# Optimization experiments

Hardware: AMD Instinct MI355X
Metric: run time of the kernel (lower is better)

## Reference

```python
import jax, jax.numpy as jnp
import numpy as np

N = 16384      # total nodes (16 graphs x 1024 nodes)
PG = 1024      # nodes per graph
NB = 16        # graphs in batch
E = 131072     # edges (intra-graph)
FIN = 16       # input_dim; xy coords in cols 0,1
HID = 128      # hidden_dim
H = 4          # num_heads
DH = HID // H  # per-head dim
NLAYERS = 3
NCLS = 1
NEG_SLOPE = 0.2

# D2 views: identity, flip-x, flip-y, flip-both (signs applied to xy cols 0,1)
_signs = np.ones((4, FIN), np.float32)
_signs[1, 0] = -1.0
_signs[2, 1] = -1.0
_signs[3, 0] = -1.0
_signs[3, 1] = -1.0
VIEW_SIGNS = jnp.asarray(_signs)


def setup_inputs() -> dict:
    key = jax.random.key(0)
    ks = jax.random.split(key, 16)
    x = jax.random.normal(ks[0], (N, FIN), jnp.float32)
    # intra-graph edges: dst forced into same graph block as src (matches the
    # torch per-graph edge filtering, which drops all cross-graph edges)
    src = jax.random.randint(ks[1], (E,), 0, N, dtype=jnp.int32)
    off = jax.random.randint(ks[2], (E,), 0, PG, dtype=jnp.int32)
    dst = (src // PG) * PG + off
    edge_index = jnp.stack([src, dst], axis=0)
    batch = (jnp.arange(N, dtype=jnp.int32) // PG)

    def w(k, fi, fo):
        return (jax.random.normal(k, (fi, fo), jnp.float32) / np.sqrt(fi))

    return dict(
        x=x, edge_index=edge_index, batch=batch,
        W0l=w(ks[3], FIN, HID), W0r=w(ks[4], FIN, HID),
        a0=jax.random.normal(ks[5], (H, DH), jnp.float32) / np.sqrt(DH),
        Wres0=w(ks[6], FIN, HID),
        Wl=jax.random.normal(ks[7], (NLAYERS - 1, HID, HID), jnp.float32) / np.sqrt(HID),
        Wr=jax.random.normal(ks[8], (NLAYERS - 1, HID, HID), jnp.float32) / np.sqrt(HID),
        att=jax.random.normal(ks[9], (NLAYERS - 1, H, DH), jnp.float32) / np.sqrt(DH),
        Wh1=w(ks[10], HID, HID), bh1=jnp.zeros((HID,), jnp.float32),
        Wh2=w(ks[11], HID, NCLS), bh2=jnp.zeros((NCLS,), jnp.float32),
    )


def _gatv2_layer(h, Wlk, Wrk, a, src, dst, Wres=None, act=True):
    # GATv2: e_ij = a^T LeakyReLU(Wl h_j + Wr h_i), softmax over incoming edges of i
    hl = (h @ Wlk).reshape(-1, H, DH)   # [N,H,D] source messages
    hr = (h @ Wrk).reshape(-1, H, DH)   # [N,H,D] target queries
    s = hl[src] + hr[dst]               # [E,H,D]
    e = jnp.einsum('ehd,hd->eh', jax.nn.leaky_relu(s, NEG_SLOPE), a)  # [E,H]
    m = jax.ops.segment_max(e, dst, num_segments=N)
    ex = jnp.exp(e - m[dst])
    denom = jax.ops.segment_sum(ex, dst, num_segments=N)
    alpha = ex / (denom[dst] + 1e-16)   # [E,H] per-dst softmax
    out = jax.ops.segment_sum(alpha[..., None] * hl[src], dst, num_segments=N)
    out = out.reshape(-1, H * DH)
    res = h @ Wres if Wres is not None else h
    out = out + res
    return jax.nn.elu(out) if act else out


def _backbone(xv, src, dst, W0l, W0r, a0, Wres0, Wl, Wr, att):
    h = _gatv2_layer(xv, W0l, W0r, a0, src, dst, Wres=Wres0, act=True)
    for i in range(NLAYERS - 1):
        last = (i == NLAYERS - 2)
        h = _gatv2_layer(h, Wl[i], Wr[i], att[i], src, dst, Wres=None, act=not last)
    return h


def reference(x, edge_index, batch, W0l, W0r, a0, Wres0, Wl, Wr, att, Wh1, bh1, Wh2, bh2):
    src, dst = edge_index[0], edge_index[1]
    # 4 D2 views of node features (sign flips on xy columns); vmap over views
    x4 = x[None, :, :] * VIEW_SIGNS[:, None, :]  # [4,N,FIN]
    emb4 = jax.vmap(lambda xv: _backbone(xv, src, dst, W0l, W0r, a0, Wres0, Wl, Wr, att))(x4)  # [4,N,HID]
    node_emb = emb4.mean(axis=0)  # mean over D2 views -> [N,HID]
    logits = jax.nn.relu(node_emb @ Wh1 + bh1) @ Wh2 + bh2  # [N,NCLS]
    return logits
```

## Files before the change

kernel.cpp:

```cpp
#include <hip/hip_runtime.h>
#include <hip/hip_bf16.h>
#include <math.h>

#define NN 16384
#define EE 131072
#define FIN 16
#define HID 128
#define NEG_SLOPE 0.2f

typedef float  floatx4 __attribute__((ext_vector_type(4)));
typedef short  shortx8 __attribute__((ext_vector_type(8)));

__device__ inline unsigned bf_hi_bits(float x) {
    unsigned u = __float_as_uint(x);
    return (u + 0x7FFFu + ((u >> 16) & 1u)) >> 16;
}

__global__ void count_kernel(const int* __restrict__ dst, int* __restrict__ deg) {
    int e = blockIdx.x * 256 + threadIdx.x;
    atomicAdd(&deg[dst[e]], 1);
}

__global__ __launch_bounds__(1024) void scan_kernel(int* __restrict__ degw ,
                                                    int* __restrict__ ptr) {
    __shared__ int sums[1024];
    int t = threadIdx.x;
    int base = t * 16;
    int local[16];
    int s = 0;
#pragma unroll
    for (int i = 0; i < 16; i++) { local[i] = degw[base + i]; s += local[i]; }
    sums[t] = s;
    __syncthreads();
    for (int off = 1; off < 1024; off <<= 1) {
        int v = (t >= off) ? sums[t - off] : 0;
        __syncthreads();
        sums[t] += v;
        __syncthreads();
    }
    int ex = (t == 0) ? 0 : sums[t - 1];
#pragma unroll
    for (int i = 0; i < 16; i++) {
        ptr[base + i] = ex;
        degw[base + i] = ex;
        ex += local[i];
    }
    if (t == 1023) ptr[NN] = sums[1023];
}

__global__ void scatter_kernel(const int* __restrict__ src, const int* __restrict__ dst,
                               int* __restrict__ ptrw, int* __restrict__ csr_src) {
    int e = blockIdx.x * 256 + threadIdx.x;
    int p = atomicAdd(&ptrw[dst[e]], 1);
    csr_src[p] = src[e];
}

__global__ void wsplit_kernel(const float* __restrict__ Wl, const float* __restrict__ Wr,
                              const float* __restrict__ Wh1,
                              unsigned short* __restrict__ hi, unsigned short* __restrict__ lo) {
    int mat = blockIdx.y;
    const float* W = (mat == 0) ? Wl : (mat == 1) ? Wr : (mat == 2) ? Wl + HID * HID
                   : (mat == 3) ? Wr + HID * HID : Wh1;
    int ct = blockIdx.x;
    int t = threadIdx.x;
    int kt = t >> 6, l = t & 63;
    long obase = (((long)mat * 32 + (ct * 4 + kt)) * 64 + l) * 8;
    int c = ct * 16 + (l & 15);
    int kbase = kt * 32 + ((l >> 4) << 3);
#pragma unroll
    for (int j = 0; j < 8; j++) {
        float x = W[(kbase + j) * HID + c];
        unsigned hb = bf_hi_bits(x);
        float r = x - __uint_as_float(hb << 16);
        unsigned lb = bf_hi_bits(r);
        hi[obase + j] = (unsigned short)hb;
        lo[obase + j] = (unsigned short)lb;
    }
}

#define L0_BLOCKS 2048
__global__ __launch_bounds__(256) void l0_kernel(const float* __restrict__ x,
                                                 const float* __restrict__ W0l,
                                                 const float* __restrict__ W0r,
                                                 const float* __restrict__ Wres,
                                                 float* __restrict__ hl,
                                                 float* __restrict__ hr,
                                                 float* __restrict__ hres,
                                                 int viewBase, long totalRows) {
    int tid = threadIdx.x;
    int c2 = (tid & 63) * 2;
    float2 wl2[FIN], wr2[FIN], ws2[FIN];
#pragma unroll
    for (int k = 0; k < FIN; k++) {
        wl2[k] = *(const float2*)(W0l + k * HID + c2);
        wr2[k] = *(const float2*)(W0r + k * HID + c2);
        ws2[k] = *(const float2*)(Wres + k * HID + c2);
    }
    for (long lw = (long)blockIdx.x * 4 + (tid >> 6); lw < totalRows;
         lw += (long)L0_BLOCKS * 4) {
        int v = viewBase + (int)(lw >> 14);
        int n = (int)(lw & (NN - 1));
        const float* xr = x + (long)n * FIN;
        float al0 = 0.f, al1 = 0.f, ar0 = 0.f, ar1 = 0.f, as0 = 0.f, as1 = 0.f;
#pragma unroll
        for (int k = 0; k < FIN; k++) {
            float xk = xr[k];
            if (k == 0 && (v & 1)) xk = -xk;
            if (k == 1 && (v & 2)) xk = -xk;
            al0 += xk * wl2[k].x; al1 += xk * wl2[k].y;
            ar0 += xk * wr2[k].x; ar1 += xk * wr2[k].y;
            as0 += xk * ws2[k].x; as1 += xk * ws2[k].y;
        }
        long base = lw * HID + c2;
        *(float2*)(hl + base)   = make_float2(al0, al1);
        *(float2*)(hr + base)   = make_float2(ar0, ar1);
        *(float2*)(hres + base) = make_float2(as0, as1);
    }
}

__global__ __launch_bounds__(256) void attn_kernel(const float* __restrict__ hl,
                                                   const float* __restrict__ hr,
                                                   const float* __restrict__ res,
                                                   const int* __restrict__ ptr,
                                                   const int* __restrict__ csr_src,
                                                   const float* __restrict__ avec,
                                                   float* __restrict__ hout,
                                                   int act,
                                                   int gvPerXcd) {
    int xcd = blockIdx.x & 7;
    int slot = blockIdx.x >> 3;
    int gv = xcd * gvPerXcd + (slot >> 8);
    int within = slot & 255;
    int gw = (gv << 10) + (within << 2) + (threadIdx.x >> 6);
    int l = threadIdx.x & 63;
    int n = gw & (NN - 1);
    int col = ((l >> 4) << 5) + ((l & 15) << 1);
    long base = (long)gw * HID;
    float2 hr2 = *(const float2*)(hr + base + col);
    float2 a2 = *(const float2*)(avec + col);
    float m = -INFINITY, ssum = 0.f, acc0 = 0.f, acc1 = 0.f;
    int beg = ptr[n], end = ptr[n + 1];
    long vbase = (long)(gw >> 14) * NN * HID;
    int j = beg;
    for (; j + 1 < end; j += 2) {
        int sa = csr_src[j];
        int sb = csr_src[j + 1];
        float2 ha = *(const float2*)(hl + vbase + (long)sa * HID + col);
        float2 hb = *(const float2*)(hl + vbase + (long)sb * HID + col);
        float sa0 = ha.x + hr2.x, sa1 = ha.y + hr2.y;
        float sb0 = hb.x + hr2.x, sb1 = hb.y + hr2.y;
        float ta0 = sa0 > 0.f ? sa0 : NEG_SLOPE * sa0;
        float ta1 = sa1 > 0.f ? sa1 : NEG_SLOPE * sa1;
        float tb0 = sb0 > 0.f ? sb0 : NEG_SLOPE * sb0;
        float tb1 = sb1 > 0.f ? sb1 : NEG_SLOPE * sb1;
        float p1 = ta0 * a2.x + ta1 * a2.y;
        float p2 = tb0 * a2.x + tb1 * a2.y;
        p1 += __shfl_xor(p1, 1, 16);
        p2 += __shfl_xor(p2, 1, 16);
        p1 += __shfl_xor(p1, 2, 16);
        p2 += __shfl_xor(p2, 2, 16);
        p1 += __shfl_xor(p1, 4, 16);
        p2 += __shfl_xor(p2, 4, 16);
        p1 += __shfl_xor(p1, 8, 16);
        p2 += __shfl_xor(p2, 8, 16);
        float m12 = fmaxf(p1, p2);
        float w1 = __expf(p1 - m12);
        float w2 = __expf(p2 - m12);
        float mn = fmaxf(m, m12);
        float cold = __expf(m - mn);
        float c12 = __expf(m12 - mn);
        ssum = ssum * cold + (w1 + w2) * c12;
        acc0 = acc0 * cold + (w1 * ha.x + w2 * hb.x) * c12;
        acc1 = acc1 * cold + (w1 * ha.y + w2 * hb.y) * c12;
        m = mn;
    }
    if (j < end) {
        int sa = csr_src[j];
        float2 ha = *(const float2*)(hl + vbase + (long)sa * HID + col);
        float s0 = ha.x + hr2.x, s1 = ha.y + hr2.y;
        float t0 = s0 > 0.f ? s0 : NEG_SLOPE * s0;
        float t1 = s1 > 0.f ? s1 : NEG_SLOPE * s1;
        float p = t0 * a2.x + t1 * a2.y;
        p += __shfl_xor(p, 1, 16);
        p += __shfl_xor(p, 2, 16);
        p += __shfl_xor(p, 4, 16);
        p += __shfl_xor(p, 8, 16);
        float mn = fmaxf(m, p);
        float cold = __expf(m - mn);
        float wnew = __expf(p - mn);
        ssum = ssum * cold + wnew;
        acc0 = acc0 * cold + wnew * ha.x;
        acc1 = acc1 * cold + wnew * ha.y;
        m = mn;
    }
    float inv = 1.f / (ssum + 1e-16f);
    float2 r2 = *(const float2*)(res + base + col);
    float o0 = acc0 * inv + r2.x;
    float o1 = acc1 * inv + r2.y;
    if (act) {
        o0 = o0 > 0.f ? o0 : expm1f(o0);
        o1 = o1 > 0.f ? o1 : expm1f(o1);
    }
    *(float2*)(hout + base + col) = make_float2(o0, o1);
}

__global__ __launch_bounds__(256) void gemm_mfma(const float* __restrict__ A,
                                                 const unsigned short* __restrict__ whi,
                                                 const unsigned short* __restrict__ wlo,
                                                 int mat0, int mat1,
                                                 float* __restrict__ C0, float* __restrict__ C1,
                                                 const float* __restrict__ bias, int doRelu) {
    int mat = (blockIdx.z == 0) ? mat0 : mat1;
    float* C = (blockIdx.z == 0) ? C0 : C1;
    const unsigned short* bh = whi + (long)mat * 16384;
    const unsigned short* bl = wlo + (long)mat * 16384;
    int tid = threadIdx.x;
    int w = tid >> 6, l = tid & 63;
    int rh = w >> 1, ch = w & 1;
    long row0 = (long)blockIdx.x * 128 + rh * 64;
    int lr = l & 15;
    int lk = (l >> 4) << 3;
    floatx4 acc[4][4];
#pragma unroll
    for (int i = 0; i < 4; i++)
#pragma unroll
        for (int j = 0; j < 4; j++) acc[i][j] = (floatx4)0.f;

    for (int kt = 0; kt < 4; kt++) {
        shortx8 bhf[4], blf[4];
#pragma unroll
        for (int ctl = 0; ctl < 4; ctl++) {
            int ct = ch * 4 + ctl;
            long fi = ((long)(ct * 4 + kt) * 64 + l) * 8;
            bhf[ctl] = *(const shortx8*)(bh + fi);
            blf[ctl] = *(const shortx8*)(bl + fi);
        }
#pragma unroll
        for (int rt = 0; rt < 4; rt++) {
            const float* ap = A + (row0 + rt * 16 + lr) * HID + kt * 32 + lk;
            float4 x0 = *(const float4*)(ap);
            float4 x1 = *(const float4*)(ap + 4);
            float xs[8] = {x0.x, x0.y, x0.z, x0.w, x1.x, x1.y, x1.z, x1.w};
            shortx8 ah, al;
#pragma unroll
            for (int i = 0; i < 8; i++) {
                unsigned hb = bf_hi_bits(xs[i]);
                float r = xs[i] - __uint_as_float(hb << 16);
                unsigned lb = bf_hi_bits(r);
                ah[i] = (short)hb;
                al[i] = (short)lb;
            }
#pragma unroll
            for (int ctl = 0; ctl < 4; ctl++)
                acc[rt][ctl] = __builtin_amdgcn_mfma_f32_16x16x32_bf16(ah, bhf[ctl], acc[rt][ctl], 0, 0, 0);
#pragma unroll
            for (int ctl = 0; ctl < 4; ctl++)
                acc[rt][ctl] = __builtin_amdgcn_mfma_f32_16x16x32_bf16(ah, blf[ctl], acc[rt][ctl], 0, 0, 0);
#pragma unroll
            for (int ctl = 0; ctl < 4; ctl++)
                acc[rt][ctl] = __builtin_amdgcn_mfma_f32_16x16x32_bf16(al, bhf[ctl], acc[rt][ctl], 0, 0, 0);
        }
    }
    int lrow4 = (l >> 4) * 4;
#pragma unroll
    for (int rt = 0; rt < 4; rt++) {
#pragma unroll
        for (int ctl = 0; ctl < 4; ctl++) {
            int col = ch * 64 + ctl * 16 + lr;
            float badd = bias ? bias[col] : 0.f;
#pragma unroll
            for (int rg = 0; rg < 4; rg++) {
                long row = row0 + rt * 16 + lrow4 + rg;
                float v = acc[rt][ctl][rg] + badd;
                if (doRelu) v = fmaxf(v, 0.f);
                C[row * HID + col] = v;
            }
        }
    }
}

__global__ void acc_kernel(const float* __restrict__ h, float* __restrict__ emb, int k) {
    int i = blockIdx.x * 256 + threadIdx.x;
    const float4* h4 = (const float4*)h;
    float4 s = make_float4(0.f, 0.f, 0.f, 0.f);
    for (int lv = 0; lv < k; lv++) {
        float4 a = h4[i + (long)lv * NN * 32];
        s.x += a.x; s.y += a.y; s.z += a.z; s.w += a.w;
    }
    float4* e4 = (float4*)emb;
    float4 o = e4[i];
    o.x += 0.25f * s.x; o.y += 0.25f * s.y; o.z += 0.25f * s.z; o.w += 0.25f * s.w;
    e4[i] = o;
}

__global__ void logits_kernel(const float* __restrict__ z, const float* __restrict__ Wh2,
                              const float* __restrict__ bh2, float* __restrict__ out) {
    int w = (blockIdx.x * 256 + threadIdx.x) >> 6;
    int l = threadIdx.x & 63;
    float v = z[(long)w * HID + l] * Wh2[l] + z[(long)w * HID + 64 + l] * Wh2[64 + l];
    v += __shfl_xor(v, 32);
    v += __shfl_xor(v, 16);
    v += __shfl_xor(v, 8);
    v += __shfl_xor(v, 4);
    v += __shfl_xor(v, 2);
    v += __shfl_xor(v, 1);
    if (l == 0) out[w] = v + bh2[0];
}

extern "C" void kernel_launch(void* const* d_in, const int* in_sizes, int n_in,
                              void* d_out, int out_size, void* d_ws, size_t ws_size,
                              hipStream_t stream) {
    const float* x    = (const float*)d_in[0];
    const int*   ei   = (const int*)d_in[1];
    const float* W0l  = (const float*)d_in[3];
    const float* W0r  = (const float*)d_in[4];
    const float* a0   = (const float*)d_in[5];
    const float* Wres0= (const float*)d_in[6];
    const float* Wl   = (const float*)d_in[7];
    const float* Wr   = (const float*)d_in[8];
    const float* att  = (const float*)d_in[9];
    const float* Wh1  = (const float*)d_in[10];
    const float* bh1  = (const float*)d_in[11];
    const float* Wh2  = (const float*)d_in[12];
    const float* bh2  = (const float*)d_in[13];
    float* out = (float*)d_out;

    const int* src = ei;
    const int* dst = ei + EE;

    char* wsb = (char*)d_ws;
    float* emb = (float*)wsb;
    size_t off = (size_t)NN * HID * 4;
    int* ptr  = (int*)(wsb + off);  off += (NN + 1) * 4;
    int* ptrw = (int*)(wsb + off);  off += NN * 4;
    int* csr  = (int*)(wsb + off);  off += (size_t)EE * 4;
    off = (off + 255) & ~(size_t)255;
    unsigned short* whi = (unsigned short*)(wsb + off); off += 5 * 16384 * 2;
    unsigned short* wlo = (unsigned short*)(wsb + off); off += 5 * 16384 * 2;
    off = (off + 255) & ~(size_t)255;
    size_t fixedBytes = off;

    int k = 4;
    while (k > 1 && fixedBytes + 3ull * k * NN * HID * 4 > ws_size) k >>= 1;
    long K = (long)k * NN;
    int npass = 4 / k;
    int gvPerXcd = (int)(K / 1024) / 8;

    float* bufA = (float*)(wsb + off);
    float* bufB = bufA + K * HID;
    float* bufC = bufB + K * HID;

    hipMemsetAsync(ptrw, 0, NN * sizeof(int), stream);
    count_kernel<<<EE / 256, 256, 0, stream>>>(dst, ptrw);
    scan_kernel<<<1, 1024, 0, stream>>>(ptrw, ptr);
    scatter_kernel<<<EE / 256, 256, 0, stream>>>(src, dst, ptrw, csr);
    wsplit_kernel<<<dim3(8, 5), 256, 0, stream>>>(Wl, Wr, Wh1, whi, wlo);

    hipMemsetAsync(emb, 0, (size_t)NN * HID * sizeof(float), stream);

    for (int p = 0; p < npass; p++) {
        int viewBase = p * k;
        l0_kernel<<<L0_BLOCKS, 256, 0, stream>>>(x, W0l, W0r, Wres0, bufA, bufB, bufC,
                                                 viewBase, K);
        attn_kernel<<<K / 4, 256, 0, stream>>>(bufA, bufB, bufC, ptr, csr, a0, bufB, 1, gvPerXcd);
        gemm_mfma<<<dim3(K / 128, 1, 2), 256, 0, stream>>>(bufB, whi, wlo, 0, 1,
                                                           bufA, bufC, nullptr, 0);
        attn_kernel<<<K / 4, 256, 0, stream>>>(bufA, bufC, bufB, ptr, csr, att, bufC, 1, gvPerXcd);
        gemm_mfma<<<dim3(K / 128, 1, 2), 256, 0, stream>>>(bufC, whi, wlo, 2, 3,
                                                           bufA, bufB, nullptr, 0);
        attn_kernel<<<K / 4, 256, 0, stream>>>(bufA, bufB, bufC, ptr, csr, att + HID, bufB, 0, gvPerXcd);
        acc_kernel<<<NN * 32 / 256, 256, 0, stream>>>(bufB, emb, k);
    }

    gemm_mfma<<<dim3(NN / 128, 1, 1), 256, 0, stream>>>(emb, whi, wlo, 4, 4,
                                                        bufA, bufA, bh1, 1);
    logits_kernel<<<NN * 64 / 256, 256, 0, stream>>>(bufA, Wh2, bh2, out);
}
```

Before: 393.3 us.

## Split attention edges across wave quarters with 8-wide per-lane features

Restructures the per-node attention kernel: each wave's 64 lanes now form 4 edge-parallel groups of 16 lanes, each lane holding 8 contiguous features (two float4 loads) instead of 2. Each group keeps its own online-softmax state over a strided subset of edges, and the groups are merged at the end with cross-lane max/rescale/sum shuffles. Head dot products reduce over 4 lanes instead of 16, which cuts shuffle traffic per edge and raises memory-level parallelism for gathers. In exchange it adds a final cross-group reduction, leaves three quarters of lanes idle during the write, and uses a fast __expf-1 for ELU in place of expm1f, which loses some precision near zero.

```diff
diff --git a/kernel.cpp b/kernel.cpp
--- a/kernel.cpp
+++ b/kernel.cpp
@@ -128,80 +128,98 @@
                                                    int act,
                                                    int gvPerXcd) {
     int xcd = blockIdx.x & 7;
-    int slot = blockIdx.x >> 3;
-    int gv = xcd * gvPerXcd + (slot >> 8);
-    int within = slot & 255;
+    int slotb = blockIdx.x >> 3;
+    int gv = xcd * gvPerXcd + (slotb >> 8);
+    int within = slotb & 255;
     int gw = (gv << 10) + (within << 2) + (threadIdx.x >> 6);
     int l = threadIdx.x & 63;
+    int es = l >> 4;
+    int col = (l & 15) * 8;
     int n = gw & (NN - 1);
-    int col = ((l >> 4) << 5) + ((l & 15) << 1);
     long base = (long)gw * HID;
-    float2 hr2 = *(const float2*)(hr + base + col);
-    float2 a2 = *(const float2*)(avec + col);
-    float m = -INFINITY, ssum = 0.f, acc0 = 0.f, acc1 = 0.f;
+    const float* hrp = hr + base + col;
+    float4 hrA = *(const float4*)(hrp);
+    float4 hrB = *(const float4*)(hrp + 4);
+    float4 aA = *(const float4*)(avec + col);
+    float4 aB = *(const float4*)(avec + col + 4);
+    float m = -INFINITY, ssum = 0.f;
+    float4 acA = make_float4(0.f, 0.f, 0.f, 0.f);
+    float4 acB = make_float4(0.f, 0.f, 0.f, 0.f);
     int beg = ptr[n], end = ptr[n + 1];
-    long vbase = (long)(gw >> 14) * NN * HID;
-    int j = beg;
-    for (; j + 1 < end; j += 2) {
-        int sa = csr_src[j];
-        int sb = csr_src[j + 1];
-        float2 ha = *(const float2*)(hl + vbase + (long)sa * HID + col);
-        float2 hb = *(const float2*)(hl + vbase + (long)sb * HID + col);
-        float sa0 = ha.x + hr2.x, sa1 = ha.y + hr2.y;
-        float sb0 = hb.x + hr2.x, sb1 = hb.y + hr2.y;
-        float ta0 = sa0 > 0.f ? sa0 : NEG_SLOPE * sa0;
-        float ta1 = sa1 > 0.f ? sa1 : NEG_SLOPE * sa1;
-        float tb0 = sb0 > 0.f ? sb0 : NEG_SLOPE * sb0;
-        float tb1 = sb1 > 0.f ? sb1 : NEG_SLOPE * sb1;
-        float p1 = ta0 * a2.x + ta1 * a2.y;
-        float p2 = tb0 * a2.x + tb1 * a2.y;
-        p1 += __shfl_xor(p1, 1, 16);
-        p2 += __shfl_xor(p2, 1, 16);
-        p1 += __shfl_xor(p1, 2, 16);
-        p2 += __shfl_xor(p2, 2, 16);
-        p1 += __shfl_xor(p1, 4, 16);
-        p2 += __shfl_xor(p2, 4, 16);
-        p1 += __shfl_xor(p1, 8, 16);
-        p2 += __shfl_xor(p2, 8, 16);
-        float m12 = fmaxf(p1, p2);
-        float w1 = __expf(p1 - m12);
-        float w2 = __expf(p2 - m12);
-        float mn = fmaxf(m, m12);
-        float cold = __expf(m - mn);
-        float c12 = __expf(m12 - mn);
-        ssum = ssum * cold + (w1 + w2) * c12;
-        acc0 = acc0 * cold + (w1 * ha.x + w2 * hb.x) * c12;
-        acc1 = acc1 * cold + (w1 * ha.y + w2 * hb.y) * c12;
-        m = mn;
-    }
-    if (j < end) {
-        int sa = csr_src[j];
-        float2 ha = *(const float2*)(hl + vbase + (long)sa * HID + col);
-        float s0 = ha.x + hr2.x, s1 = ha.y + hr2.y;
-        float t0 = s0 > 0.f ? s0 : NEG_SLOPE * s0;
-        float t1 = s1 > 0.f ? s1 : NEG_SLOPE * s1;
-        float p = t0 * a2.x + t1 * a2.y;
-        p += __shfl_xor(p, 1, 16);
-        p += __shfl_xor(p, 2, 16);
-        p += __shfl_xor(p, 4, 16);
-        p += __shfl_xor(p, 8, 16);
+    const float* hlv = hl + (long)(gw >> 14) * NN * HID;
+
+    for (int j = beg + es; j < end; j += 4) {
+        int sn = csr_src[j];
+        const float* hp = hlv + ((sn << 7) + col);
+        float4 hA = *(const float4*)(hp);
+        float4 hB = *(const float4*)(hp + 4);
+        float p;
+        {
+            float s0 = hA.x + hrA.x, s1 = hA.y + hrA.y, s2 = hA.z + hrA.z, s3 = hA.w + hrA.w;
+            float s4 = hB.x + hrB.x, s5 = hB.y + hrB.y, s6 = hB.z + hrB.z, s7 = hB.w + hrB.w;
+            float t0 = fmaxf(s0, 0.f) + NEG_SLOPE * fminf(s0, 0.f);
+            float t1 = fmaxf(s1, 0.f) + NEG_SLOPE * fminf(s1, 0.f);
+            float t2 = fmaxf(s2, 0.f) + NEG_SLOPE * fminf(s2, 0.f);
+            float t3 = fmaxf(s3, 0.f) + NEG_SLOPE * fminf(s3, 0.f);
+            float t4 = fmaxf(s4, 0.f) + NEG_SLOPE * fminf(s4, 0.f);
+            float t5 = fmaxf(s5, 0.f) + NEG_SLOPE * fminf(s5, 0.f);
+            float t6 = fmaxf(s6, 0.f) + NEG_SLOPE * fminf(s6, 0.f);
+            float t7 = fmaxf(s7, 0.f) + NEG_SLOPE * fminf(s7, 0.f);
+            p = t0 * aA.x + t1 * aA.y + t2 * aA.z + t3 * aA.w
+              + t4 * aB.x + t5 * aB.y + t6 * aB.z + t7 * aB.w;
+        }
+        p += __shfl_xor(p, 1, 4);
+        p += __shfl_xor(p, 2, 4);
         float mn = fmaxf(m, p);
         float cold = __expf(m - mn);
-        float wnew = __expf(p - mn);
-        ssum = ssum * cold + wnew;
-        acc0 = acc0 * cold + wnew * ha.x;
-        acc1 = acc1 * cold + wnew * ha.y;
+        float w = __expf(p - mn);
+        ssum = ssum * cold + w;
+        acA.x = acA.x * cold + w * hA.x;
+        acA.y = acA.y * cold + w * hA.y;
+        acA.z = acA.z * cold + w * hA.z;
+        acA.w = acA.w * cold + w * hA.w;
+        acB.x = acB.x * cold + w * hB.x;
+        acB.y = acB.y * cold + w * hB.y;
+        acB.z = acB.z * cold + w * hB.z;
+        acB.w = acB.w * cold + w * hB.w;
         m = mn;
     }
-    float inv = 1.f / (ssum + 1e-16f);
-    float2 r2 = *(const float2*)(res + base + col);
-    float o0 = acc0 * inv + r2.x;
-    float o1 = acc1 * inv + r2.y;
-    if (act) {
-        o0 = o0 > 0.f ? o0 : expm1f(o0);
-        o1 = o1 > 0.f ? o1 : expm1f(o1);
-    }
-    *(float2*)(hout + base + col) = make_float2(o0, o1);
+
+    float mG = fmaxf(m, __shfl_xor(m, 16));
+    mG = fmaxf(mG, __shfl_xor(mG, 32));
+    float sc = (m > -INFINITY) ? __expf(m - mG) : 0.f;
+    ssum *= sc;
+    acA.x *= sc; acA.y *= sc; acA.z *= sc; acA.w *= sc;
+    acB.x *= sc; acB.y *= sc; acB.z *= sc; acB.w *= sc;
+    ssum += __shfl_xor(ssum, 16); ssum += __shfl_xor(ssum, 32);
+    acA.x += __shfl_xor(acA.x, 16); acA.x += __shfl_xor(acA.x, 32);
+    acA.y += __shfl_xor(acA.y, 16); acA.y += __shfl_xor(acA.y, 32);
+    acA.z += __shfl_xor(acA.z, 16); acA.z += __shfl_xor(acA.z, 32);
+    acA.w += __shfl_xor(acA.w, 16); acA.w += __shfl_xor(acA.w, 32);
+    acB.x += __shfl_xor(acB.x, 16); acB.x += __shfl_xor(acB.x, 32);
+    acB.y += __shfl_xor(acB.y, 16); acB.y += __shfl_xor(acB.y, 32);
+    acB.z += __shfl_xor(acB.z, 16); acB.z += __shfl_xor(acB.z, 32);
+    acB.w += __shfl_xor(acB.w, 16); acB.w += __shfl_xor(acB.w, 32);
+
+    if (es == 0) {
+        float inv = 1.f / (ssum + 1e-16f);
+        const float* rp = res + base + col;
+        float4 rA = *(const float4*)(rp);
+        float4 rB = *(const float4*)(rp + 4);
+        float o[8];
+        o[0] = acA.x * inv + rA.x; o[1] = acA.y * inv + rA.y;
+        o[2] = acA.z * inv + rA.z; o[3] = acA.w * inv + rA.w;
+        o[4] = acB.x * inv + rB.x; o[5] = acB.y * inv + rB.y;
+        o[6] = acB.z * inv + rB.z; o[7] = acB.w * inv + rB.w;
+        if (act) {
+#pragma unroll
+            for (int i = 0; i < 8; i++)
+                o[i] = o[i] > 0.f ? o[i] : (__expf(o[i]) - 1.f);
+        }
+        float* op = hout + base + col;
+        *(float4*)(op)     = make_float4(o[0], o[1], o[2], o[3]);
+        *(float4*)(op + 4) = make_float4(o[4], o[5], o[6], o[7]);
+    }
 }
 
 __global__ __launch_bounds__(256) void gemm_mfma(const float* __restrict__ A,
```

After: 361.5 us. 1.09x faster.
